# Optimization experiments

Measured on AMD Instinct MI355X. Metric: run time of the kernel, lower is better.

## Reference

```python
import math
import jax, jax.numpy as jnp
import numpy as np

NH = 16          # num_attention_heads
MAX_REL = 512    # max_relative_positions


def _t4(x):
    # [B, N, H] -> [B, NH, N, H/NH]  (transpose_for_scores)
    B, N, H = x.shape
    return x.reshape(B, N, NH, -1).transpose(0, 2, 1, 3)


def setup_inputs() -> dict:
    key = jax.random.key(0)
    ks = jax.random.split(key, 6)
    B, N, H = 1, 2048, 1024
    hidden_states = jax.random.normal(ks[0], (B, N, H), jnp.float32)
    attention_mask = jnp.ones((B, 1, N, N), jnp.int32)
    ids = jnp.arange(N, dtype=jnp.int32)
    relative_pos = ids[:, None] - ids[None, :]              # [N, N], build_relative_position
    rel_embeddings = jax.random.normal(ks[1], (2 * MAX_REL, H), jnp.float32) * 0.02
    in_proj_w = jax.random.normal(ks[2], (3 * H, H), jnp.float32) * 0.02
    q_bias = jnp.zeros((H,), jnp.float32)
    v_bias = jnp.zeros((H,), jnp.float32)
    pos_proj_w = jax.random.normal(ks[3], (H, H), jnp.float32) * 0.02
    pos_q_proj_w = jax.random.normal(ks[4], (H, H), jnp.float32) * 0.02
    pos_q_proj_b = jnp.zeros((H,), jnp.float32)
    return dict(hidden_states=hidden_states, attention_mask=attention_mask,
                relative_pos=relative_pos, rel_embeddings=rel_embeddings,
                in_proj_w=in_proj_w, q_bias=q_bias, v_bias=v_bias,
                pos_proj_w=pos_proj_w, pos_q_proj_w=pos_q_proj_w,
                pos_q_proj_b=pos_q_proj_b)


def reference(hidden_states, attention_mask, relative_pos, rel_embeddings,
              in_proj_w, q_bias, v_bias, pos_proj_w, pos_q_proj_w, pos_q_proj_b):
    B, N, H = hidden_states.shape
    dh = H // NH
    scale_factor = 1 + 2  # 1 + len(["c2p", "p2c"])
    scale = math.sqrt(dh * scale_factor)

    # fused QKV projection; chunk(3, dim=-1) AFTER transpose_for_scores -> per-head q|k|v layout
    qp = hidden_states @ in_proj_w.T                          # [B, N, 3H]
    q, k, v = jnp.split(_t4(qp), 3, axis=-1)                  # each [B, NH, N, dh]
    q = q + _t4(q_bias[None, None, :])
    v = v + _t4(v_bias[None, None, :])
    q = q / scale

    scores = jnp.einsum('bhqd,bhkd->bhqk', q, k)              # content-content

    # disentangled relative-position bias
    span = min(N, MAX_REL)                                    # att_span
    rel = rel_embeddings[MAX_REL - span:MAX_REL + span][None] # [1, 2S, H]
    rpos = relative_pos.astype(jnp.int32)[None, None]         # [1, 1, N, N]

    # c2p: content-to-position
    pos_k = _t4(rel @ pos_proj_w.T)                           # [1, NH, 2S, dh]
    c2p = jnp.einsum('bhqd,xhsd->bhqs', q, pos_k)             # [B, NH, N, 2S]
    c2p_pos = jnp.clip(rpos + span, 0, 2 * span - 1)
    c2p = jnp.take_along_axis(c2p, c2p_pos, axis=-1)          # gather -> [B, NH, N, N]

    # p2c: position-to-content
    pos_q = _t4(rel @ pos_q_proj_w.T + pos_q_proj_b) / scale  # [1, NH, 2S, dh]
    p2c = jnp.einsum('bhkd,xhsd->bhks', k, pos_q)             # [B, NH, N, 2S]
    p2c_pos = jnp.clip(-rpos + span, 0, 2 * span - 1)
    p2c = jnp.take_along_axis(p2c, p2c_pos, axis=-1)          # [B, NH, K, Q]
    p2c = jnp.swapaxes(p2c, -1, -2)                           # -> [B, NH, Q, K]

    scores = scores + c2p + p2c

    # XSoftmax: masked softmax, masked probs zeroed
    m = attention_mask.astype(bool)                           # [B, 1, N, N]
    probs = jax.nn.softmax(jnp.where(m, scores, -jnp.inf), axis=-1)
    probs = jnp.where(m, probs, 0.0)

    ctx = jnp.einsum('bhqk,bhkd->bhqd', probs, v)             # [B, NH, N, dh]
    return ctx.transpose(0, 2, 1, 3).reshape(B, N, H)
```

## Files before the change

### kernel.cpp

```cpp
#include <hip/hip_runtime.h>
#include <hip/hip_bf16.h>

typedef __bf16 bf16;
typedef __attribute__((ext_vector_type(8))) __bf16 bf16x8;
typedef __attribute__((ext_vector_type(8))) float f32x8;
typedef __attribute__((ext_vector_type(4))) float f32x4;

#define MFMA(a,b,c) __builtin_amdgcn_mfma_f32_16x16x32_bf16((a),(b),(c),0,0,0)

__device__ __forceinline__ bf16x8 ld8(const bf16* p){ bf16x8 v; __builtin_memcpy(&v,p,16); return v; }
__device__ __forceinline__ void   st8(bf16* p, bf16x8 v){ __builtin_memcpy(p,&v,16); }

__global__ __launch_bounds__(256)
void cvt_kernel(const float* __restrict__ s0, const float* __restrict__ s1,
                const float* __restrict__ s2, const float* __restrict__ s3,
                const float* __restrict__ s4,
                bf16* d0, bf16* d1, bf16* d2, bf16* d3, bf16* d4)
{
    const int sizes[5] = {2097152, 3145728, 1048576, 1048576, 1048576};
    const float* s; bf16* d;
    switch (blockIdx.y) {
        case 0: s = s0; d = d0; break;  case 1: s = s1; d = d1; break;
        case 2: s = s2; d = d2; break;  case 3: s = s3; d = d3; break;
        default: s = s4; d = d4;
    }
    const int n = sizes[blockIdx.y];
    const int stride = gridDim.x * 256 * 8;
    for (int i = (blockIdx.x * 256 + threadIdx.x) * 8; i < n; i += stride) {
        f32x8 v; __builtin_memcpy(&v, s + i, 32);
        bf16x8 r;
        #pragma unroll
        for (int j = 0; j < 8; j++) r[j] = (bf16)v[j];
        st8(d + i, r);
    }
}

__global__ __launch_bounds__(256)
void gemm_stage(const bf16* __restrict__ A, const bf16* __restrict__ Bpk,
                const bf16* __restrict__ Bpq, int K, int mode,
                const float* __restrict__ qb, const float* __restrict__ vb,
                bf16* __restrict__ o0, bf16* __restrict__ o1, bf16* __restrict__ o2,
                float* __restrict__ part)
{
    __shared__ __attribute__((aligned(16))) bf16 As[128][32];
    __shared__ __attribute__((aligned(16))) bf16 Bs[128][32];

    const int tid = threadIdx.x, w = tid >> 6, lane = tid & 63;
    const int l15 = lane & 15, quad = lane >> 4;
    const int wr = w >> 1, wc = w & 1;

    int arr = 0, my = blockIdx.y, kbeg = 0, kend = K;
    const bf16* B = Bpk;
    if (mode == 1) {
        arr = my >> 3; my &= 7;
        B = arr ? Bpq : Bpk;
        kbeg = blockIdx.z * 256; kend = kbeg + 256;
    }
    const int m0 = my * 128, n0 = blockIdx.x * 128;
    const int srow = tid >> 2, scol = (tid & 3) * 8;

    f32x4 acc[4][4] = {};
    for (int k0 = kbeg; k0 < kend; k0 += 32) {
        __syncthreads();
        st8(&As[srow][scol],    ld8(A + (size_t)(m0 + srow) * K + k0 + scol));
        st8(&As[srow+64][scol], ld8(A + (size_t)(m0 + 64 + srow) * K + k0 + scol));
        st8(&Bs[srow][scol],    ld8(B + (size_t)(n0 + srow) * K + k0 + scol));
        st8(&Bs[srow+64][scol], ld8(B + (size_t)(n0 + 64 + srow) * K + k0 + scol));
        __syncthreads();
        bf16x8 a[4], b[4];
        #pragma unroll
        for (int i = 0; i < 4; i++) a[i] = ld8(&As[wr*64 + i*16 + l15][quad*8]);
        #pragma unroll
        for (int j = 0; j < 4; j++) b[j] = ld8(&Bs[wc*64 + j*16 + l15][quad*8]);
        #pragma unroll
        for (int i = 0; i < 4; i++)
            #pragma unroll
            for (int j = 0; j < 4; j++)
                acc[i][j] = MFMA(a[i], b[j], acc[i][j]);
    }

    const float inv_scale = 0.07216878364870323f;
    #pragma unroll
    for (int i = 0; i < 4; i++) {
        #pragma unroll
        for (int j = 0; j < 4; j++) {
            #pragma unroll
            for (int r = 0; r < 4; r++) {
                int row = m0 + wr*64 + i*16 + quad*4 + r;
                int col = n0 + wc*64 + j*16 + l15;
                float v = acc[i][j][r];
                if (mode == 0) {
                    int h = col / 192, rr = col % 192;
                    if (rr < 64)
                        o0[((size_t)h*2048 + row)*64 + rr] =
                            (bf16)((v + qb[h*64 + rr]) * inv_scale);
                    else if (rr < 128)
                        o1[((size_t)h*2048 + row)*64 + (rr - 64)] = (bf16)v;
                    else
                        o2[((size_t)h*64 + (rr - 128))*2048 + row] =
                            (bf16)(v + vb[h*64 + (rr - 128)]);
                } else {
                    part[(((size_t)(arr*4 + blockIdx.z)*1024 + row)*1024) + col] = v;
                }
            }
        }
    }
}

__global__ __launch_bounds__(256)
void pos_merge(const float* __restrict__ part, const float* __restrict__ pqb,
               bf16* __restrict__ PKw, bf16* __restrict__ PQw)
{
    int e = blockIdx.x * 256 + threadIdx.x;
    int arr = e >> 20, r = (e >> 10) & 1023, c = e & 1023;
    const float* p = part + ((size_t)arr*4) * 1048576 + (size_t)r * 1024 + c;
    float v = p[0] + p[1048576] + p[2*1048576] + p[3*1048576];
    int h = c >> 6, d = c & 63;
    if (arr == 0) PKw[((size_t)h*1024 + r)*64 + d] = (bf16)v;
    else          PQw[((size_t)h*1024 + r)*64 + d] =
                      (bf16)((v + pqb[c]) * 0.07216878364870323f);
}

__global__ __launch_bounds__(256)
void pos_tab(const bf16* __restrict__ Kw, const bf16* __restrict__ PQw,
             bf16* __restrict__ T)
{
    __shared__ __attribute__((aligned(16))) bf16 As[128][32];
    __shared__ __attribute__((aligned(16))) bf16 Bs[128][32];

    const int tid = threadIdx.x, w = tid >> 6, lane = tid & 63;
    const int l15 = lane & 15, quad = lane >> 4;
    const int wr = w >> 1, wc = w & 1;
    const int h = blockIdx.z;
    const int m0 = blockIdx.y * 128, n0 = blockIdx.x * 128;
    const bf16* A = Kw  + (size_t)h * 2048 * 64;
    const bf16* B = PQw + (size_t)h * 1024 * 64;
    const int srow = tid >> 2, scol = (tid & 3) * 8;

    f32x4 acc[4][4] = {};
    for (int k0 = 0; k0 < 64; k0 += 32) {
        __syncthreads();
        st8(&As[srow][scol],    ld8(A + (size_t)(m0 + srow) * 64 + k0 + scol));
        st8(&As[srow+64][scol], ld8(A + (size_t)(m0 + 64 + srow) * 64 + k0 + scol));
        st8(&Bs[srow][scol],    ld8(B + (size_t)(n0 + srow) * 64 + k0 + scol));
        st8(&Bs[srow+64][scol], ld8(B + (size_t)(n0 + 64 + srow) * 64 + k0 + scol));
        __syncthreads();
        bf16x8 a[4], b[4];
        #pragma unroll
        for (int i = 0; i < 4; i++) a[i] = ld8(&As[wr*64 + i*16 + l15][quad*8]);
        #pragma unroll
        for (int j = 0; j < 4; j++) b[j] = ld8(&Bs[wc*64 + j*16 + l15][quad*8]);
        #pragma unroll
        for (int i = 0; i < 4; i++)
            #pragma unroll
            for (int j = 0; j < 4; j++)
                acc[i][j] = MFMA(a[i], b[j], acc[i][j]);
    }

    bf16* Th = T + (size_t)h * 2048 * 1024;
    #pragma unroll
    for (int i = 0; i < 4; i++)
        #pragma unroll
        for (int j = 0; j < 4; j++)
            #pragma unroll
            for (int r = 0; r < 4; r++)
                Th[(size_t)(m0 + wr*64 + i*16 + quad*4 + r) * 1024
                   + n0 + wc*64 + j*16 + l15] = (bf16)acc[i][j][r];
}

__global__ __launch_bounds__(256)
void edge_kernel(const bf16* __restrict__ Qw, const bf16* __restrict__ Kw,
                 const bf16* __restrict__ PKw, const bf16* __restrict__ PQw,
                 float* __restrict__ C2Pe, float* __restrict__ P2Ce)
{
    int t = blockIdx.x * 256 + threadIdx.x;
    int side = t >> 15, rest = t & 32767;
    int h = rest >> 11, n = rest & 2047;
    const bf16* row = (side ? Kw : Qw) + ((size_t)h*2048 + n) * 64;
    const bf16* eb  = (side ? PQw : PKw) + (size_t)h*1024*64;
    float a0 = 0.f, a1 = 0.f;
    #pragma unroll
    for (int c = 0; c < 8; c++) {
        bf16x8 x  = ld8(row + c*8);
        bf16x8 e0 = ld8(eb + c*8);
        bf16x8 e1 = ld8(eb + (size_t)1023*64 + c*8);
        #pragma unroll
        for (int j = 0; j < 8; j++) {
            a0 += (float)x[j] * (float)e0[j];
            a1 += (float)x[j] * (float)e1[j];
        }
    }
    float* o = side ? P2Ce : C2Pe;
    o[((size_t)h*2048 + n)*2 + 0] = a0;
    o[((size_t)h*2048 + n)*2 + 1] = a1;
}

#define KSPLIT 2

__global__ __launch_bounds__(64, 4)
void attn_kernel(const bf16* __restrict__ Q, const bf16* __restrict__ Kc,
                 const bf16* __restrict__ Vt, const bf16* __restrict__ PK,
                 const bf16* __restrict__ P2Ct,
                 const float* __restrict__ C2Pe, const float* __restrict__ P2Ce,
                 float* __restrict__ opart, float* __restrict__ pspart)
{
    __shared__ bf16 W1s[16][82];
    __shared__ __attribute__((aligned(16))) bf16 Ps[16][72];

    const int lane = threadIdx.x;
    const int l15 = lane & 15, quad = lane >> 4;
    const int h = blockIdx.y, qw0 = blockIdx.x * 16, z = blockIdx.z;

    const bf16* Qh  = Q  + (size_t)h * 2048 * 64;
    const bf16* Kh  = Kc + (size_t)h * 2048 * 64;
    const bf16* Vh  = Vt + (size_t)h * 64 * 2048;
    const bf16* PKh = PK + (size_t)h * 1024 * 64;
    const bf16* Pth = P2Ct + (size_t)h * 2048 * 1024;

    bf16x8 qa[2];
    #pragma unroll
    for (int s = 0; s < 2; s++)
        qa[s] = ld8(Qh + (size_t)(qw0 + l15)*64 + s*32 + quad*8);

    f32x4 oacc[4] = {};
    float psum[4] = {0.f, 0.f, 0.f, 0.f};

    for (int i = 0; i < 32 / KSPLIT; i++) {
        const int kb = z + i * KSPLIT;
        const int k0 = kb * 64;

        bf16x8 kf[4][2];
        #pragma unroll
        for (int nt = 0; nt < 4; nt++)
            #pragma unroll
            for (int s = 0; s < 2; s++)
                kf[nt][s] = ld8(Kh + (size_t)(k0 + nt*16 + l15)*64 + s*32 + quad*8);

        f32x4 sacc[4] = {};
        #pragma unroll
        for (int s = 0; s < 2; s++)
            #pragma unroll
            for (int nt = 0; nt < 4; nt++)
                sacc[nt] = MFMA(qa[s], kf[nt][s], sacc[nt]);

        if (k0 >= qw0 + 527) {
            float ce[4];
            #pragma unroll
            for (int r = 0; r < 4; r++)
                ce[r] = C2Pe[((size_t)h*2048 + qw0 + quad*4 + r)*2 + 0];
            #pragma unroll
            for (int nt = 0; nt < 4; nt++) {
                float p2 = P2Ce[((size_t)h*2048 + k0 + nt*16 + l15)*2 + 0];
                #pragma unroll
                for (int r = 0; r < 4; r++)
                    sacc[nt][r] += ce[r] + p2;
            }
        } else if (k0 <= qw0 - 574) {
            float ce[4];
            #pragma unroll
            for (int r = 0; r < 4; r++)
                ce[r] = C2Pe[((size_t)h*2048 + qw0 + quad*4 + r)*2 + 1];
            #pragma unroll
            for (int nt = 0; nt < 4; nt++) {
                float p2 = P2Ce[((size_t)h*2048 + k0 + nt*16 + l15)*2 + 1];
                #pragma unroll
                for (int r = 0; r < 4; r++)
                    sacc[nt][r] += ce[r] + p2;
            }
        } else {
            const int winb = qw0 - k0 + 449;
            {
                f32x4 a1[5] = {};
                #pragma unroll
                for (int s = 0; s < 2; s++)
                    #pragma unroll
                    for (int n5 = 0; n5 < 5; n5++) {
                        int c = winb + n5*16 + l15;
                        c = min(max(c, 0), 1023);
                        bf16x8 bq = ld8(PKh + (size_t)c*64 + s*32 + quad*8);
                        a1[n5] = MFMA(qa[s], bq, a1[n5]);
                    }
                #pragma unroll
                for (int n5 = 0; n5 < 5; n5++)
                    #pragma unroll
                    for (int r = 0; r < 4; r++)
                        W1s[quad*4 + r][n5*16 + l15] = (bf16)a1[n5][r];
            }
            #pragma unroll
            for (int nt = 0; nt < 4; nt++) {
                const bf16* prow = Pth + (size_t)(k0 + nt*16 + l15) * 1024;
                #pragma unroll
                for (int r = 0; r < 4; r++) {
                    int off = quad*4 + r - nt*16 - l15 + 63;
                    int idx = min(max(winb + off, 0), 1023);
                    sacc[nt][r] += (float)W1s[quad*4 + r][off]
                                 + (float)prow[idx];
                }
            }
        }

        #pragma unroll
        for (int nt = 0; nt < 4; nt++)
            #pragma unroll
            for (int r = 0; r < 4; r++) {
                float e = __expf(sacc[nt][r]);
                psum[r] += e;
                Ps[quad*4 + r][nt*16 + l15] = (bf16)e;
            }

        #pragma unroll
        for (int s = 0; s < 2; s++) {
            bf16x8 pa = ld8(&Ps[l15][s*32 + quad*8]);
            #pragma unroll
            for (int dt = 0; dt < 4; dt++) {
                bf16x8 vf = ld8(Vh + (size_t)(dt*16 + l15)*2048 + k0 + s*32 + quad*8);
                oacc[dt] = MFMA(pa, vf, oacc[dt]);
            }
        }
    }

    #pragma unroll
    for (int r = 0; r < 4; r++)
        #pragma unroll
        for (int m = 1; m < 16; m <<= 1)
            psum[r] += __shfl_xor(psum[r], m);

    const size_t zb = (size_t)(z * 16 + h);
    #pragma unroll
    for (int dt = 0; dt < 4; dt++)
        #pragma unroll
        for (int r = 0; r < 4; r++) {
            int row = qw0 + quad*4 + r;
            opart[(zb*2048 + row)*64 + dt*16 + l15] = oacc[dt][r];
        }
    if (l15 == 0) {
        #pragma unroll
        for (int r = 0; r < 4; r++)
            pspart[zb*2048 + qw0 + quad*4 + r] = psum[r];
    }
}

__global__ __launch_bounds__(256)
void attn_merge(const float* __restrict__ opart, const float* __restrict__ pspart,
                float* __restrict__ out)
{
    int t = blockIdx.x * 256 + threadIdx.x;
    int row = t >> 10, c = t & 1023, h = c >> 6, d = c & 63;
    float o = 0.f, p = 0.f;
    #pragma unroll
    for (int zz = 0; zz < KSPLIT; zz++) {
        size_t zb = (size_t)(zz * 16 + h);
        o += opart[(zb*2048 + row)*64 + d];
        p += pspart[zb*2048 + row];
    }
    out[t] = o / p;
}

extern "C" void kernel_launch(void* const* d_in, const int* in_sizes, int n_in,
                              void* d_out, int out_size, void* d_ws, size_t ws_size,
                              hipStream_t stream)
{
    (void)in_sizes; (void)n_in; (void)out_size; (void)ws_size;
    const float* X   = (const float*)d_in[0];
    const float* REL = (const float*)d_in[3];
    const float* Win = (const float*)d_in[4];
    const float* qb  = (const float*)d_in[5];
    const float* vb  = (const float*)d_in[6];
    const float* Wpk = (const float*)d_in[7];
    const float* Wpq = (const float*)d_in[8];
    const float* pqb = (const float*)d_in[9];
    float* out = (float*)d_out;

    char* ws = (char*)d_ws;
    const size_t MB = 1024u * 1024u;
    bf16*  Xb    = (bf16*)(ws);
    bf16*  Winb  = (bf16*)(ws + 4*MB);
    bf16*  Wpkb  = (bf16*)(ws + 10*MB);
    bf16*  Wpqb  = (bf16*)(ws + 12*MB);
    bf16*  RELb  = (bf16*)(ws + 14*MB);
    bf16*  Qw    = (bf16*)(ws + 16*MB);
    bf16*  Kw    = (bf16*)(ws + 20*MB);
    bf16*  Vtw   = (bf16*)(ws + 24*MB);
    bf16*  PKw   = (bf16*)(ws + 28*MB);
    bf16*  PQw   = (bf16*)(ws + 30*MB);
    float* Ppart = (float*)(ws + 32*MB);
    bf16*  P2Ct  = (bf16*)(ws + 32*MB);
    float* C2Pe  = (float*)(ws + 96*MB);
    float* P2Ce  = (float*)(ws + 96*MB + 256*1024);
    float* Opart  = (float*)(ws);
    float* PSpart = (float*)(ws + 96*MB + 512*1024);

    cvt_kernel<<<dim3(1536, 5), 256, 0, stream>>>(X, Win, Wpk, Wpq, REL,
                                                  Xb, Winb, Wpkb, Wpqb, RELb);
    gemm_stage<<<dim3(24, 16, 1), 256, 0, stream>>>(Xb, Winb, Winb, 1024, 0,
                                                    qb, vb, Qw, Kw, Vtw, nullptr);
    gemm_stage<<<dim3(8, 16, 4), 256, 0, stream>>>(RELb, Wpkb, Wpqb, 1024, 1,
                                                   nullptr, nullptr,
                                                   nullptr, nullptr, nullptr, Ppart);
    pos_merge<<<dim3(8192), 256, 0, stream>>>(Ppart, pqb, PKw, PQw);
    pos_tab<<<dim3(8, 16, 16), 256, 0, stream>>>(Kw, PQw, P2Ct);
    edge_kernel<<<dim3(256), 256, 0, stream>>>(Qw, Kw, PKw, PQw, C2Pe, P2Ce);
    attn_kernel<<<dim3(128, 16, KSPLIT), 64, 0, stream>>>(Qw, Kw, Vtw, PKw, P2Ct,
                                                          C2Pe, P2Ce, Opart, PSpart);
    attn_merge<<<dim3(8192), 256, 0, stream>>>(Opart, PSpart, out);
}
```

Before: 402.8 us.

## Store p2c table skewed by query index so attention reads contiguous rows

pos_tab now stages its output tile in shared memory and writes it diagonally into a table indexed by query row instead of key row. The attention kernel can then read p2c bias values from one row per query with nearby offsets rather than gathering across 64 key rows. Out-of-range window positions fall back to the precomputed edge values. The diagonal write loop is serial per thread and leaves parts of the table unwritten, trading write efficiency for better read locality in attention.

```diff
diff --git a/kernel.cpp b/kernel.cpp
--- a/kernel.cpp
+++ b/kernel.cpp
@@ -123,10 +123,12 @@
 
 __global__ __launch_bounds__(256)
 void pos_tab(const bf16* __restrict__ Kw, const bf16* __restrict__ PQw,
-             bf16* __restrict__ T)
-{
-    __shared__ __attribute__((aligned(16))) bf16 As[128][32];
-    __shared__ __attribute__((aligned(16))) bf16 Bs[128][32];
+             bf16* __restrict__ Tq)
+{
+    __shared__ __attribute__((aligned(16))) char smem[128 * 130 * 2];
+    bf16 (*As)[32]  = (bf16(*)[32])smem;
+    bf16 (*Bs)[32]  = (bf16(*)[32])(smem + 8192);
+    bf16 (*Ts)[130] = (bf16(*)[130])smem;
 
     const int tid = threadIdx.x, w = tid >> 6, lane = tid & 63;
     const int l15 = lane & 15, quad = lane >> 4;
@@ -157,15 +159,24 @@
                 acc[i][j] = MFMA(a[i], b[j], acc[i][j]);
     }
 
-    bf16* Th = T + (size_t)h * 2048 * 1024;
+    __syncthreads();
     #pragma unroll
     for (int i = 0; i < 4; i++)
         #pragma unroll
         for (int j = 0; j < 4; j++)
             #pragma unroll
             for (int r = 0; r < 4; r++)
-                Th[(size_t)(m0 + wr*64 + i*16 + quad*4 + r) * 1024
-                   + n0 + wc*64 + j*16 + l15] = (bf16)acc[i][j][r];
+                Ts[wr*64 + i*16 + quad*4 + r][wc*64 + j*16 + l15] =
+                    (bf16)acc[i][j][r];
+    __syncthreads();
+
+    const int q = m0 + n0 - 512 + tid;
+    if (tid < 255 && q >= 0 && q < 2048) {
+        bf16* dst = Tq + (size_t)h * 2048 * 1024 + (size_t)q * 1024 + n0;
+        const int lo = max(0, tid - 127), hi = min(127, tid);
+        for (int cc = lo; cc <= hi; ++cc)
+            dst[cc] = Ts[tid - cc][cc];
+    }
 }
 
 __global__ __launch_bounds__(256)
@@ -200,7 +211,7 @@
 __global__ __launch_bounds__(64, 4)
 void attn_kernel(const bf16* __restrict__ Q, const bf16* __restrict__ Kc,
                  const bf16* __restrict__ Vt, const bf16* __restrict__ PK,
-                 const bf16* __restrict__ P2Ct,
+                 const bf16* __restrict__ Tq,
                  const float* __restrict__ C2Pe, const float* __restrict__ P2Ce,
                  float* __restrict__ opart, float* __restrict__ pspart)
 {
@@ -215,7 +226,7 @@
     const bf16* Kh  = Kc + (size_t)h * 2048 * 64;
     const bf16* Vh  = Vt + (size_t)h * 64 * 2048;
     const bf16* PKh = PK + (size_t)h * 1024 * 64;
-    const bf16* Pth = P2Ct + (size_t)h * 2048 * 1024;
+    const bf16* Tqh = Tq + (size_t)h * 2048 * 1024;
 
     bf16x8 qa[2];
     #pragma unroll
@@ -286,15 +297,35 @@
                     for (int r = 0; r < 4; r++)
                         W1s[quad*4 + r][n5*16 + l15] = (bf16)a1[n5][r];
             }
-            #pragma unroll
-            for (int nt = 0; nt < 4; nt++) {
-                const bf16* prow = Pth + (size_t)(k0 + nt*16 + l15) * 1024;
+            if (winb >= 0 && winb <= 945) {
                 #pragma unroll
                 for (int r = 0; r < 4; r++) {
-                    int off = quad*4 + r - nt*16 - l15 + 63;
-                    int idx = min(max(winb + off, 0), 1023);
-                    sacc[nt][r] += (float)W1s[quad*4 + r][off]
-                                 + (float)prow[idx];
+                    const bf16* trow = Tqh + (size_t)(qw0 + quad*4 + r) * 1024;
+                    const int base = winb + quad*4 + r + 63 - l15;
+                    #pragma unroll
+                    for (int nt = 0; nt < 4; nt++) {
+                        int off = base - winb - nt*16;
+                        sacc[nt][r] += (float)W1s[quad*4 + r][off]
+                                     + (float)trow[base - nt*16];
+                    }
+                }
+            } else {
+                #pragma unroll
+                for (int nt = 0; nt < 4; nt++) {
+                    const int k = k0 + nt*16 + l15;
+                    #pragma unroll
+                    for (int r = 0; r < 4; r++) {
+                        int off = quad*4 + r - nt*16 - l15 + 63;
+                        int cc  = winb + off;
+                        float pv;
+                        if (cc < 0)
+                            pv = P2Ce[((size_t)h*2048 + k)*2 + 0];
+                        else if (cc > 1023)
+                            pv = P2Ce[((size_t)h*2048 + k)*2 + 1];
+                        else
+                            pv = (float)Tqh[(size_t)(qw0 + quad*4 + r)*1024 + cc];
+                        sacc[nt][r] += (float)W1s[quad*4 + r][off] + pv;
+                    }
                 }
             }
         }
@@ -384,7 +415,7 @@
     bf16*  PKw   = (bf16*)(ws + 28*MB);
     bf16*  PQw   = (bf16*)(ws + 30*MB);
     float* Ppart = (float*)(ws + 32*MB);
-    bf16*  P2Ct  = (bf16*)(ws + 32*MB);
+    bf16*  Tq    = (bf16*)(ws + 32*MB);
     float* C2Pe  = (float*)(ws + 96*MB);
     float* P2Ce  = (float*)(ws + 96*MB + 256*1024);
     float* Opart  = (float*)(ws);
@@ -398,9 +429,9 @@
                                                    nullptr, nullptr,
                                                    nullptr, nullptr, nullptr, Ppart);
     pos_merge<<<dim3(8192), 256, 0, stream>>>(Ppart, pqb, PKw, PQw);
-    pos_tab<<<dim3(8, 16, 16), 256, 0, stream>>>(Kw, PQw, P2Ct);
+    pos_tab<<<dim3(8, 16, 16), 256, 0, stream>>>(Kw, PQw, Tq);
     edge_kernel<<<dim3(256), 256, 0, stream>>>(Qw, Kw, PKw, PQw, C2Pe, P2Ce);
-    attn_kernel<<<dim3(128, 16, KSPLIT), 64, 0, stream>>>(Qw, Kw, Vtw, PKw, P2Ct,
+    attn_kernel<<<dim3(128, 16, KSPLIT), 64, 0, stream>>>(Qw, Kw, Vtw, PKw, Tq,
                                                           C2Pe, P2Ce, Opart, PSpart);
     attn_merge<<<dim3(8192), 256, 0, stream>>>(Opart, PSpart, out);
 }
```

Result: no change. 405.4 us (+0.6%).
